# Kernel tuning notes

Measured on AMD Instinct MI355X. Metric: run time of the kernel, lower is better.

Reference implementation:

```python
import jax, jax.numpy as jnp
import numpy as np

N = 100000   # nodes
E = 400000   # edges
R = 237      # relations
D = 200      # feature dim (dims=[200,200,200])
B = 4096     # triple batch
L = 2        # num GAT layers
ALPHA = 0.01 # leaky-relu slope


def setup_inputs() -> dict:
    key = jax.random.key(0)
    ks = jax.random.split(key, 11)
    return dict(
        ent_embed=jax.random.normal(ks[0], (N, D), jnp.float32),
        rel_embed=jax.random.normal(ks[1], (R, D), jnp.float32),
        W_gat=jax.random.normal(ks[2], (L, D, D), jnp.float32) * 0.1,
        att_a=jax.random.normal(ks[3], (L, 2 * D), jnp.float32) * 0.1,
        W_hw=jax.random.normal(ks[4], (D, D), jnp.float32) * 0.1,
        b_hw=jax.random.normal(ks[5], (1, D), jnp.float32) * 0.1,
        edge_src=jax.random.randint(ks[6], (E,), 0, N),
        edge_dst=jax.random.randint(ks[7], (E,), 0, N),
        batch_h=jax.random.randint(ks[8], (B,), 0, N),
        batch_r=jax.random.randint(ks[9], (B,), 0, R),
        batch_t=jax.random.randint(ks[10], (B,), 0, N),
    )


def _gat_layer(x, W, a, src, dst):
    # x: [N,D], W: [D,D], a: [2D]
    Wh = x @ W                                  # [N,D]
    s_src = Wh @ a[:D]                          # [N] source score
    s_dst = Wh @ a[D:]                          # [N] dest score
    e = jax.nn.leaky_relu(s_src[src] + s_dst[dst], ALPHA)  # [E]
    # segment softmax over incoming edges of each destination node
    m = jax.ops.segment_max(e, dst, num_segments=N)
    m = jax.lax.stop_gradient(jnp.where(jnp.isfinite(m), m, 0.0))
    ex = jnp.exp(e - m[dst])
    denom = jax.ops.segment_sum(ex, dst, num_segments=N)
    att = ex / jnp.maximum(denom[dst], 1e-9)    # [E]
    out = jax.ops.segment_sum(att[:, None] * Wh[src], dst, num_segments=N)  # [N,D]
    return jax.nn.sigmoid(out)                  # act = torch.sigmoid, 1 head, concat=False


def reference(ent_embed, rel_embed, W_gat, att_a, W_hw, b_hw,
              edge_src, edge_dst, batch_h, batch_r, batch_t):
    x = ent_embed
    for i in range(L):
        gat_out = _gat_layer(x, W_gat[i], att_a[i], edge_src, edge_dst)
        # highway gate: sigma = sigmoid(x W + b); shared W,b across layers
        sigma = jax.nn.sigmoid(x @ W_hw + b_hw)
        x = sigma * gat_out + (1.0 - sigma) * x
    h = x[batch_h]
    r = rel_embed[batch_r]
    t = x[batch_t]
    return (h, r, t)
```

## Files before the change

kernel.cpp:

```cpp
#include <hip/hip_runtime.h>
#include <math.h>

#define NNODES 100000
#define NEDGES 400000
#define DIM    200
#define NB     4096
#define NL     2
#define ALPHA  0.01f
#define D4     (DIM/4)
#define NPAD   100096
#define KPAD   224
#define NKS    7
#define NCF    26
#define NBB    (2*NB)
#define NBLK   ((NNODES + 255) / 256)
#define SCAN_BPB 1024
#define NSB    ((NNODES + SCAN_BPB - 1) / SCAN_BPB)
#define GFULL  (NPAD / 32)
#define GEMM_TOT (2 * GFULL)
#define SLICE  ((GEMM_TOT + 3) / 4)
#define CSBLK  ((NPAD * 32) / 256)
#define HBLK   ((NEDGES + 255) / 256)
#define PREPBLK ((2 * NKS * NCF * 64 + NL * 2 * DIM + 255) / 256)
#define SCATB  ((NEDGES + 447) / 448)
#define MARKB  ((NBB + 447) / 448)
#define SGB    (NBB / 32)
#define RELB   ((NB * D4 + 447) / 448)

typedef __attribute__((ext_vector_type(8))) short short8;
typedef __attribute__((ext_vector_type(4))) float f32x4;

__device__ __forceinline__ float sigm(float v) { return 1.0f / (1.0f + expf(-v)); }
__device__ __forceinline__ unsigned short f2bf(float f) {
    unsigned u = __float_as_uint(f);
    unsigned r = u + 0x7fff + ((u >> 16) & 1);
    return (unsigned short)(r >> 16);
}
__device__ __forceinline__ float bflo(unsigned u) { return __uint_as_float(u << 16); }
__device__ __forceinline__ float bfhi(unsigned u) { return __uint_as_float(u & 0xffff0000u); }

template<int MODE>
__device__ void scan_body(const int* __restrict__ in, int* __restrict__ state,
                          int* __restrict__ ticket, int* __restrict__ o0,
                          int* __restrict__ o1, int* __restrict__ o2, int tid)
{
    __shared__ int sbid;
    __shared__ int tmp[256];
    __shared__ int sexcl;
    if (tid == 0) sbid = atomicAdd(ticket, 1);
    __syncthreads();
    int bid = sbid;
    int base = bid * SCAN_BPB + tid * 4;

    int4 v4 = make_int4(0, 0, 0, 0);
    if (tid < 256) {
        if (base + 3 < NNODES) v4 = *(const int4*)(in + base);
        else {
            if (base + 0 < NNODES) v4.x = in[base + 0];
            if (base + 1 < NNODES) v4.y = in[base + 1];
            if (base + 2 < NNODES) v4.z = in[base + 2];
        }
    }
    int s1 = v4.x + v4.y, s2 = s1 + v4.z, s3 = s2 + v4.w;

    if (tid < 256) tmp[tid] = s3;
    __syncthreads();
#pragma unroll
    for (int off = 1; off < 256; off <<= 1) {
        int t = (tid < 256 && tid >= off) ? tmp[tid - off] : 0;
        __syncthreads();
        if (tid < 256) tmp[tid] += t;
        __syncthreads();
    }
    int bexcl_t = (tid < 256) ? (tmp[tid] - s3) : 0;
    int btotal  = tmp[255];

    if (tid == 0) {
        int st = (bid == 0) ? ((2 << 30) | btotal) : ((1 << 30) | btotal);
        __hip_atomic_store(&state[bid], st, __ATOMIC_RELEASE, __HIP_MEMORY_SCOPE_AGENT);
        if (bid == 0) sexcl = 0;
    }
    if (bid > 0 && tid < 64) {
        int excl = 0;
        int pred = bid - 1;
        while (pred >= -64) {
            int idx = pred - tid;
            int s = (idx >= 0)
                ? __hip_atomic_load(&state[idx], __ATOMIC_ACQUIRE, __HIP_MEMORY_SCOPE_AGENT)
                : (2 << 30);
            int f = ((unsigned)s) >> 30;
            unsigned long long nv = __ballot(f == 0);
            unsigned long long iv = __ballot(f == 2);
            int firstnv = nv ? (__ffsll(nv) - 1) : 64;
            int firstiv = iv ? (__ffsll(iv) - 1) : 64;
            if (firstiv < firstnv) {
                int contrib = (tid <= firstiv) ? (s & 0x3FFFFFFF) : 0;
#pragma unroll
                for (int m = 32; m; m >>= 1) contrib += __shfl_xor(contrib, m, 64);
                excl += contrib;
                break;
            } else if (firstnv > 0) {
                int contrib = (tid < firstnv) ? (s & 0x3FFFFFFF) : 0;
#pragma unroll
                for (int m = 32; m; m >>= 1) contrib += __shfl_xor(contrib, m, 64);
                excl += contrib;
                pred -= firstnv;
            }
        }
        if (tid == 0) {
            __hip_atomic_store(&state[bid], (2 << 30) | (excl + btotal),
                               __ATOMIC_RELEASE, __HIP_MEMORY_SCOPE_AGENT);
            sexcl = excl;
        }
    }
    __syncthreads();
    int ex = sexcl + bexcl_t;

    if (tid < 256) {
        if (MODE == 0) {
            int4 r = make_int4(ex, ex + v4.x, ex + s1, ex + s2);
            if (base + 3 < NNODES) {
                *(int4*)(o0 + base) = r;
                *(int4*)(o1 + base) = r;
            } else {
                if (base + 0 < NNODES) { o0[base + 0] = r.x; o1[base + 0] = r.x; }
                if (base + 1 < NNODES) { o0[base + 1] = r.y; o1[base + 1] = r.y; }
                if (base + 2 < NNODES) { o0[base + 2] = r.z; o1[base + 2] = r.z; }
            }
            if (bid == NSB - 1 && tid == 0) o0[NNODES] = NEDGES;
        } else {
            int vv[4] = { v4.x, v4.y, v4.z, v4.w };
            int ee[4] = { ex, ex + v4.x, ex + s1, ex + s2 };
#pragma unroll
            for (int j = 0; j < 4; ++j) {
                int idx = base + j;
                if (idx < NNODES) {
                    if (vv[j]) { o0[ee[j]] = idx; o1[idx] = ee[j]; }
                    if (idx == NNODES - 1) *o2 = ee[j] + vv[j];
                }
            }
        }
    }
}

template<int CFBASE, int IND>
__device__ __forceinline__ void gemm_body(const unsigned short* __restrict__ Apack,
                                          const unsigned short* __restrict__ Wpack,
                                          const float* __restrict__ bhw,
                                          unsigned short* __restrict__ outb,
                                          const int* __restrict__ Lrow,
                                          const int* __restrict__ bh,
                                          const int* __restrict__ bt,
                                          int nrows, int vb, int tid)
{
    int rowbase = vb * 32;
    if (rowbase >= nrows) return;

    int w = tid >> 6;
    int l = tid & 63;
    int cgrp = l >> 4, cidx = l & 15;
    int cf0 = CFBASE + 2 * w;
    int cf1 = CFBASE + 2 * w + 1;
    int cf1l = (cf1 < NCF) ? cf1 : (NCF - 1);

    const short8* Bp = (const short8*)Wpack + l;
    short8 b0[NKS], b1[NKS];
#pragma unroll
    for (int ks = 0; ks < NKS; ++ks) {
        b0[ks] = Bp[(ks * NCF + cf0) * 64];
        b1[ks] = Bp[(ks * NCF + cf1l) * 64];
    }

    int e0 = rowbase + cidx, e1 = rowbase + 16 + cidx;
    int ar0, ar1;
    if (IND == 1) {
        ar0 = Lrow[min(e0, nrows - 1)];
        ar1 = Lrow[min(e1, nrows - 1)];
    } else if (IND == 2) {
        int c0 = min(e0, nrows - 1), c1 = min(e1, nrows - 1);
        ar0 = (c0 < NB) ? bh[c0] : bt[c0 - NB];
        ar1 = (c1 < NB) ? bh[c1] : bt[c1 - NB];
    } else { ar0 = e0; ar1 = e1; }

    const short8* Ap0 = (const short8*)(Apack + (size_t)ar0 * KPAD + cgrp * 8);
    const short8* Ap1 = (const short8*)(Apack + (size_t)ar1 * KPAD + cgrp * 8);

    f32x4 acc00 = (f32x4){0.f,0.f,0.f,0.f}, acc01 = acc00, acc10 = acc00, acc11 = acc00;

    short8 a0[2], a1[2];
    a0[0] = Ap0[0];
    a1[0] = Ap1[0];

#pragma unroll
    for (int ks = 0; ks < NKS; ++ks) {
        const int cur = ks & 1, nxt = cur ^ 1;
        if (ks + 1 < NKS) {
            a0[nxt] = Ap0[(ks + 1) * 4];
            a1[nxt] = Ap1[(ks + 1) * 4];
        }
        acc00 = __builtin_amdgcn_mfma_f32_16x16x32_bf16(a0[cur], b0[ks], acc00, 0, 0, 0);
        acc01 = __builtin_amdgcn_mfma_f32_16x16x32_bf16(a0[cur], b1[ks], acc01, 0, 0, 0);
        acc10 = __builtin_amdgcn_mfma_f32_16x16x32_bf16(a1[cur], b0[ks], acc10, 0, 0, 0);
        acc11 = __builtin_amdgcn_mfma_f32_16x16x32_bf16(a1[cur], b1[ks], acc11, 0, 0, 0);
    }

#pragma unroll
    for (int cc = 0; cc < 2; ++cc) {
        int cf = cc ? cf1 : cf0;
        if (cf >= CFBASE + 13) continue;
        int col = (cf - CFBASE) * 16 + cidx;
        if (col >= DIM) continue;
        f32x4 ar_0 = cc ? acc01 : acc00;
        f32x4 ar_1 = cc ? acc11 : acc10;
        if (CFBASE == 0) {
#pragma unroll
            for (int r = 0; r < 4; ++r) {
                int row = rowbase + cgrp * 4 + r;
                if (row < nrows) outb[(size_t)row * DIM + col] = f2bf(ar_0[r]);
                row += 16;
                if (row < nrows) outb[(size_t)row * DIM + col] = f2bf(ar_1[r]);
            }
        } else {
            float bb2 = bhw[col];
#pragma unroll
            for (int r = 0; r < 4; ++r) {
                int row = rowbase + cgrp * 4 + r;
                if (row < nrows) outb[(size_t)row * DIM + col] = f2bf(sigm(ar_0[r] + bb2));
                row += 16;
                if (row < nrows) outb[(size_t)row * DIM + col] = f2bf(sigm(ar_1[r] + bb2));
            }
        }
    }
}

__global__ __launch_bounds__(256) void zeroprep_k(int* __restrict__ deg, int* __restrict__ mask,
                                                  int* __restrict__ lbbuf,
                                                  const float* __restrict__ Wg,
                                                  const float* __restrict__ Whw,
                                                  const float* __restrict__ aa,
                                                  unsigned short* __restrict__ wp0,
                                                  unsigned short* __restrict__ wp1,
                                                  float* __restrict__ wv)
{
    int bid = blockIdx.x, tid = threadIdx.x;
    if (bid < NBLK) {
        int i = bid * 256 + tid;
        if (i < NNODES) { deg[i] = 0; mask[i] = 0; }
        if (i < 320) lbbuf[i] = 0;
        return;
    }
    int t0 = (bid - NBLK) * 256 + tid;
    const int WP = NKS * NCF * 64;
    if (t0 < 2 * WP) {
        int pk = (t0 >= WP) ? 1 : 0;
        int t = t0 - pk * WP;
        const float* Wgl = Wg + (size_t)pk * DIM * DIM;
        unsigned short* wp = pk ? wp1 : wp0;
        int l = t & 63, cf = (t >> 6) % NCF, ks = t / (NCF * 64);
        int col = (cf % 13) * 16 + (l & 15);
        const float* W = (cf < 13) ? Wgl : Whw;
        unsigned rr[4];
#pragma unroll
        for (int j = 0; j < 4; ++j) {
            int ka = ks * 32 + (l >> 4) * 8 + 2 * j;
            float fa = (ka < DIM && col < DIM) ? W[ka * DIM + col] : 0.f;
            float fb = (ka + 1 < DIM && col < DIM) ? W[(ka + 1) * DIM + col] : 0.f;
            rr[j] = (unsigned)f2bf(fa) | ((unsigned)f2bf(fb) << 16);
        }
        ((uint4*)wp)[t] = make_uint4(rr[0], rr[1], rr[2], rr[3]);
    } else {
        int u = t0 - 2 * WP;
        if (u >= NL * 2 * DIM) return;
        int l = u / (2 * DIM), sd = (u / DIM) % 2, k = u % DIM;
        const float* W = Wg + (size_t)l * DIM * DIM + (size_t)k * DIM;
        const float* av = aa + (size_t)l * 2 * DIM + sd * DIM;
        float s = 0.f;
        for (int c = 0; c < DIM; ++c) s = fmaf(W[c], av[c], s);
        wv[u] = s;
    }
}

__global__ __launch_bounds__(256) void convhist_k(const float* __restrict__ xin,
                                                  const float* __restrict__ wvl,
                                                  unsigned short* __restrict__ ap,
                                                  float* __restrict__ s_src,
                                                  float* __restrict__ s_dst,
                                                  const int* __restrict__ edst,
                                                  int* __restrict__ deg)
{
    int bid = blockIdx.x, tid = threadIdx.x;
    if (bid >= CSBLK) {
        int e = (bid - CSBLK) * 256 + tid;
        if (e < NEDGES) atomicAdd(&deg[edst[e]], 1);
        return;
    }
    int gt = bid * 256 + tid;
    int row = gt >> 5, hl = gt & 31;

    float ps = 0.f, pd = 0.f;
    if (hl < 28) {
        uint4 o = make_uint4(0u, 0u, 0u, 0u);
        if (row < NNODES && hl < 25) {
            size_t base = (size_t)row * D4 + hl * 2;
            float4 x0 = ((const float4*)xin)[base];
            float4 x1 = ((const float4*)xin)[base + 1];
            o.x = (unsigned)f2bf(x0.x) | ((unsigned)f2bf(x0.y) << 16);
            o.y = (unsigned)f2bf(x0.z) | ((unsigned)f2bf(x0.w) << 16);
            o.z = (unsigned)f2bf(x1.x) | ((unsigned)f2bf(x1.y) << 16);
            o.w = (unsigned)f2bf(x1.z) | ((unsigned)f2bf(x1.w) << 16);
            float4 s0 = ((const float4*)wvl)[hl * 2];
            float4 s1 = ((const float4*)wvl)[hl * 2 + 1];
            float4 d0 = ((const float4*)(wvl + DIM))[hl * 2];
            float4 d1 = ((const float4*)(wvl + DIM))[hl * 2 + 1];
            ps = x0.x*s0.x + x0.y*s0.y + x0.z*s0.z + x0.w*s0.w
               + x1.x*s1.x + x1.y*s1.y + x1.z*s1.z + x1.w*s1.w;
            pd = x0.x*d0.x + x0.y*d0.y + x0.z*d0.z + x0.w*d0.w
               + x1.x*d1.x + x1.y*d1.y + x1.z*d1.z + x1.w*d1.w;
        }
        ((uint4*)ap)[(size_t)row * 28 + hl] = o;
    }
#pragma unroll
    for (int m = 16; m; m >>= 1) {
        ps += __shfl_xor(ps, m, 32);
        pd += __shfl_xor(pd, m, 32);
    }
    if (hl == 0 && row < NNODES) { s_src[row] = ps; s_dst[row] = pd; }
}

template<int PHASE>
__global__ __launch_bounds__(448) void carrier_k(const int* __restrict__ sin,
                                                 int* __restrict__ state,
                                                 int* __restrict__ ticket,
                                                 int* __restrict__ so0,
                                                 int* __restrict__ so1,
                                                 int* __restrict__ so2,
                                                 const int* __restrict__ esrc,
                                                 const int* __restrict__ edst,
                                                 int* __restrict__ cursor,
                                                 int* __restrict__ csr_src,
                                                 const int* __restrict__ bh,
                                                 const int* __restrict__ bt,
                                                 const int* __restrict__ rs,
                                                 int* __restrict__ mask,
                                                 const unsigned short* __restrict__ Apack,
                                                 const unsigned short* __restrict__ Wpack,
                                                 const float* __restrict__ bhw,
                                                 unsigned short* __restrict__ whb,
                                                 unsigned short* __restrict__ sgc,
                                                 int nsmall)
{
    int bid = blockIdx.x, tid = threadIdx.x;
    if (bid < nsmall) {
        if (PHASE == 0) {
            scan_body<0>(sin, state, ticket, so0, so1, so2, tid);
        } else if (PHASE == 3) {
            scan_body<1>(sin, state, ticket, so0, so1, so2, tid);
        } else if (PHASE == 1) {
            int e = bid * 448 + tid;
            if (e < NEDGES) {
                int d = edst[e];
                int p = atomicAdd(&cursor[d], 1);
                csr_src[p] = esrc[e];
            }
        } else {
            int e = bid * 448 + tid;
            if (e < NBB) {
                int node = (e < NB) ? bh[e] : bt[e - NB];
                mask[node] = 1;
                int b = rs[node], en = rs[node + 1];
                for (int j = b; j < en; ++j) mask[csr_src[j]] = 1;
            }
        }
        return;
    }
    int vb = PHASE * SLICE + (bid - nsmall);
    if (vb >= GEMM_TOT) return;
    if (vb < GFULL)
        gemm_body<0, 0>(Apack, Wpack, bhw, whb, nullptr, nullptr, nullptr, NNODES, vb, tid);
    else
        gemm_body<13, 0>(Apack, Wpack, bhw, sgc, nullptr, nullptr, nullptr, NNODES, vb - GFULL, tid);
}

__global__ __launch_bounds__(256) void agg3c_k(const int* __restrict__ csr_src,
                                               const int* __restrict__ rs,
                                               const float* __restrict__ s_src,
                                               const float* __restrict__ s_dst,
                                               const unsigned short* __restrict__ whb,
                                               const unsigned short* __restrict__ sgc,
                                               unsigned short* __restrict__ apack,
                                               const int* __restrict__ Lrow,
                                               const int* __restrict__ nLp,
                                               const float* __restrict__ wvn,
                                               float* __restrict__ o_ssrc,
                                               float* __restrict__ o_sdst)
{
    int gt = blockIdx.x * 256 + threadIdx.x;
    int lidx = gt >> 5;
    int hl = gt & 31;
    if (lidx >= *nLp) return;
    int node = Lrow[lidx];

    int beg = rs[node], end = rs[node + 1];
    float sd = s_dst[node];

    float m = -3.4e38f;
    for (int j = beg + hl; j < end; j += 32) {
        float v = s_src[csr_src[j]] + sd;
        v = v > 0.f ? v : ALPHA * v;
        m = fmaxf(m, v);
    }
#pragma unroll
    for (int s = 16; s; s >>= 1) m = fmaxf(m, __shfl_xor(m, s, 32));
    float sum = 0.f;
    for (int j = beg + hl; j < end; j += 32) {
        float v = s_src[csr_src[j]] + sd;
        v = v > 0.f ? v : ALPHA * v;
        sum += expf(v - m);
    }
#pragma unroll
    for (int s = 16; s; s >>= 1) sum += __shfl_xor(sum, s, 32);
    float inv_ = 1.f / fmaxf(sum, 1e-9f);

    float ps = 0.f, pd = 0.f;
    if (hl < 25) {
        float av[8] = {0.f, 0.f, 0.f, 0.f, 0.f, 0.f, 0.f, 0.f};
        int j = beg;
        for (; j + 1 < end; j += 2) {
            int n0 = csr_src[j], n1 = csr_src[j + 1];
            float v0 = s_src[n0] + sd, v1 = s_src[n1] + sd;
            v0 = v0 > 0.f ? v0 : ALPHA * v0;
            v1 = v1 > 0.f ? v1 : ALPHA * v1;
            float c0 = expf(v0 - m) * inv_, c1 = expf(v1 - m) * inv_;
            uint4 w0 = ((const uint4*)whb)[(size_t)n0 * 25 + hl];
            uint4 w1 = ((const uint4*)whb)[(size_t)n1 * 25 + hl];
            av[0] = fmaf(c0, bflo(w0.x), av[0]); av[0] = fmaf(c1, bflo(w1.x), av[0]);
            av[1] = fmaf(c0, bfhi(w0.x), av[1]); av[1] = fmaf(c1, bfhi(w1.x), av[1]);
            av[2] = fmaf(c0, bflo(w0.y), av[2]); av[2] = fmaf(c1, bflo(w1.y), av[2]);
            av[3] = fmaf(c0, bfhi(w0.y), av[3]); av[3] = fmaf(c1, bfhi(w1.y), av[3]);
            av[4] = fmaf(c0, bflo(w0.z), av[4]); av[4] = fmaf(c1, bflo(w1.z), av[4]);
            av[5] = fmaf(c0, bfhi(w0.z), av[5]); av[5] = fmaf(c1, bfhi(w1.z), av[5]);
            av[6] = fmaf(c0, bflo(w0.w), av[6]); av[6] = fmaf(c1, bflo(w1.w), av[6]);
            av[7] = fmaf(c0, bfhi(w0.w), av[7]); av[7] = fmaf(c1, bfhi(w1.w), av[7]);
        }
        if (j < end) {
            int n0 = csr_src[j];
            float v0 = s_src[n0] + sd;
            v0 = v0 > 0.f ? v0 : ALPHA * v0;
            float c0 = expf(v0 - m) * inv_;
            uint4 w0 = ((const uint4*)whb)[(size_t)n0 * 25 + hl];
            av[0] = fmaf(c0, bflo(w0.x), av[0]);
            av[1] = fmaf(c0, bfhi(w0.x), av[1]);
            av[2] = fmaf(c0, bflo(w0.y), av[2]);
            av[3] = fmaf(c0, bfhi(w0.y), av[3]);
            av[4] = fmaf(c0, bflo(w0.z), av[4]);
            av[5] = fmaf(c0, bfhi(w0.z), av[5]);
            av[6] = fmaf(c0, bflo(w0.w), av[6]);
            av[7] = fmaf(c0, bfhi(w0.w), av[7]);
        }

        uint4 sv = ((const uint4*)sgc)[(size_t)node * 25 + hl];
        uint4 xv = ((const uint4*)apack)[(size_t)node * 28 + hl];
        float4 o0, o1;
        float s0;
        s0 = bflo(sv.x); o0.x = s0 * sigm(av[0]) + (1.f - s0) * bflo(xv.x);
        s0 = bfhi(sv.x); o0.y = s0 * sigm(av[1]) + (1.f - s0) * bfhi(xv.x);
        s0 = bflo(sv.y); o0.z = s0 * sigm(av[2]) + (1.f - s0) * bflo(xv.y);
        s0 = bfhi(sv.y); o0.w = s0 * sigm(av[3]) + (1.f - s0) * bfhi(xv.y);
        s0 = bflo(sv.z); o1.x = s0 * sigm(av[4]) + (1.f - s0) * bflo(xv.z);
        s0 = bfhi(sv.z); o1.y = s0 * sigm(av[5]) + (1.f - s0) * bfhi(xv.z);
        s0 = bflo(sv.w); o1.z = s0 * sigm(av[6]) + (1.f - s0) * bflo(xv.w);
        s0 = bfhi(sv.w); o1.w = s0 * sigm(av[7]) + (1.f - s0) * bfhi(xv.w);

        unsigned r0 = (unsigned)f2bf(o0.x) | ((unsigned)f2bf(o0.y) << 16);
        unsigned r1 = (unsigned)f2bf(o0.z) | ((unsigned)f2bf(o0.w) << 16);
        unsigned r2 = (unsigned)f2bf(o1.x) | ((unsigned)f2bf(o1.y) << 16);
        unsigned r3 = (unsigned)f2bf(o1.z) | ((unsigned)f2bf(o1.w) << 16);
        ((uint4*)apack)[(size_t)node * 28 + hl] = make_uint4(r0, r1, r2, r3);

        float4 ws0 = ((const float4*)wvn)[hl * 2];
        float4 ws1 = ((const float4*)wvn)[hl * 2 + 1];
        float4 wd0 = ((const float4*)(wvn + DIM))[hl * 2];
        float4 wd1 = ((const float4*)(wvn + DIM))[hl * 2 + 1];
        ps = o0.x*ws0.x + o0.y*ws0.y + o0.z*ws0.z + o0.w*ws0.w
           + o1.x*ws1.x + o1.y*ws1.y + o1.z*ws1.z + o1.w*ws1.w;
        pd = o0.x*wd0.x + o0.y*wd0.y + o0.z*wd0.z + o0.w*wd0.w
           + o1.x*wd1.x + o1.y*wd1.y + o1.z*wd1.z + o1.w*wd1.w;
    }
#pragma unroll
    for (int s = 16; s; s >>= 1) {
        ps += __shfl_xor(ps, s, 32);
        pd += __shfl_xor(pd, s, 32);
    }
    if (hl == 0) { o_ssrc[node] = ps; o_sdst[node] = pd; }
}

__global__ __launch_bounds__(448) void l1pack_k(const unsigned short* __restrict__ Apack,
                                                const unsigned short* __restrict__ Wpack1,
                                                const float* __restrict__ bhw,
                                                unsigned short* __restrict__ whc,
                                                unsigned short* __restrict__ sgbatch,
                                                const int* __restrict__ Lrow,
                                                const int* __restrict__ nLp,
                                                const int* __restrict__ bh,
                                                const int* __restrict__ bt,
                                                const float* __restrict__ rel,
                                                const int* __restrict__ br,
                                                float* __restrict__ out)
{
    int bid = blockIdx.x, tid = threadIdx.x;
    if (bid < GFULL) {
        gemm_body<0, 1>(Apack, Wpack1, bhw, whc, Lrow, nullptr, nullptr, *nLp, bid, tid);
    } else if (bid < GFULL + SGB) {
        gemm_body<13, 2>(Apack, Wpack1, bhw, sgbatch, nullptr, bh, bt, NBB, bid - GFULL, tid);
    } else {
        int u = (bid - GFULL - SGB) * 448 + tid;
        if (u < NB * D4) {
            int row = u / D4, c = u - row * D4;
            ((float4*)out)[(size_t)(NB + row) * D4 + c] =
                ((const float4*)rel)[(size_t)br[row] * D4 + c];
        }
    }
}

__global__ __launch_bounds__(256) void agg4_k(const int* __restrict__ csr_src,
                                              const int* __restrict__ rs,
                                              const float* __restrict__ s_src,
                                              const float* __restrict__ s_dst,
                                              const unsigned short* __restrict__ whc,
                                              const int* __restrict__ inv,
                                              const unsigned short* __restrict__ sgbatch,
                                              const unsigned short* __restrict__ apack,
                                              const int* __restrict__ bh,
                                              const int* __restrict__ bt,
                                              float* __restrict__ out)
{
    int gt = blockIdx.x * 256 + threadIdx.x;
    int e = gt >> 5;
    int hl = gt & 31;
    if (e >= NBB) return;
    int node = (e < NB) ? bh[e] : bt[e - NB];
    int orow = (e < NB) ? e : (2 * NB + (e - NB));

    int beg = rs[node], end = rs[node + 1];
    float sd = s_dst[node];

    float m = -3.4e38f;
    for (int j = beg + hl; j < end; j += 32) {
        float v = s_src[csr_src[j]] + sd;
        v = v > 0.f ? v : ALPHA * v;
        m = fmaxf(m, v);
    }
#pragma unroll
    for (int s = 16; s; s >>= 1) m = fmaxf(m, __shfl_xor(m, s, 32));
    float sum = 0.f;
    for (int j = beg + hl; j < end; j += 32) {
        float v = s_src[csr_src[j]] + sd;
        v = v > 0.f ? v : ALPHA * v;
        sum += expf(v - m);
    }
#pragma unroll
    for (int s = 16; s; s >>= 1) sum += __shfl_xor(sum, s, 32);
    float inv_ = 1.f / fmaxf(sum, 1e-9f);

    if (hl < 25) {
        float av[8] = {0.f, 0.f, 0.f, 0.f, 0.f, 0.f, 0.f, 0.f};
        int j = beg;
        for (; j + 1 < end; j += 2) {
            int n0 = csr_src[j], n1 = csr_src[j + 1];
            float v0 = s_src[n0] + sd, v1 = s_src[n1] + sd;
            v0 = v0 > 0.f ? v0 : ALPHA * v0;
            v1 = v1 > 0.f ? v1 : ALPHA * v1;
            float c0 = expf(v0 - m) * inv_, c1 = expf(v1 - m) * inv_;
            uint4 w0 = ((const uint4*)whc)[(size_t)inv[n0] * 25 + hl];
            uint4 w1 = ((const uint4*)whc)[(size_t)inv[n1] * 25 + hl];
            av[0] = fmaf(c0, bflo(w0.x), av[0]); av[0] = fmaf(c1, bflo(w1.x), av[0]);
            av[1] = fmaf(c0, bfhi(w0.x), av[1]); av[1] = fmaf(c1, bfhi(w1.x), av[1]);
            av[2] = fmaf(c0, bflo(w0.y), av[2]); av[2] = fmaf(c1, bflo(w1.y), av[2]);
            av[3] = fmaf(c0, bfhi(w0.y), av[3]); av[3] = fmaf(c1, bfhi(w1.y), av[3]);
            av[4] = fmaf(c0, bflo(w0.z), av[4]); av[4] = fmaf(c1, bflo(w1.z), av[4]);
            av[5] = fmaf(c0, bfhi(w0.z), av[5]); av[5] = fmaf(c1, bfhi(w1.z), av[5]);
            av[6] = fmaf(c0, bflo(w0.w), av[6]); av[6] = fmaf(c1, bflo(w1.w), av[6]);
            av[7] = fmaf(c0, bfhi(w0.w), av[7]); av[7] = fmaf(c1, bfhi(w1.w), av[7]);
        }
        if (j < end) {
            int n0 = csr_src[j];
            float v0 = s_src[n0] + sd;
            v0 = v0 > 0.f ? v0 : ALPHA * v0;
            float c0 = expf(v0 - m) * inv_;
            uint4 w0 = ((const uint4*)whc)[(size_t)inv[n0] * 25 + hl];
            av[0] = fmaf(c0, bflo(w0.x), av[0]);
            av[1] = fmaf(c0, bfhi(w0.x), av[1]);
            av[2] = fmaf(c0, bflo(w0.y), av[2]);
            av[3] = fmaf(c0, bfhi(w0.y), av[3]);
            av[4] = fmaf(c0, bflo(w0.z), av[4]);
            av[5] = fmaf(c0, bfhi(w0.z), av[5]);
            av[6] = fmaf(c0, bflo(w0.w), av[6]);
            av[7] = fmaf(c0, bfhi(w0.w), av[7]);
        }

        uint4 sv = ((const uint4*)sgbatch)[(size_t)e * 25 + hl];
        uint4 xv = ((const uint4*)apack)[(size_t)node * 28 + hl];
        float4 o0, o1;
        float s0;
        s0 = bflo(sv.x); o0.x = s0 * sigm(av[0]) + (1.f - s0) * bflo(xv.x);
        s0 = bfhi(sv.x); o0.y = s0 * sigm(av[1]) + (1.f - s0) * bfhi(xv.x);
        s0 = bflo(sv.y); o0.z = s0 * sigm(av[2]) + (1.f - s0) * bflo(xv.y);
        s0 = bfhi(sv.y); o0.w = s0 * sigm(av[3]) + (1.f - s0) * bfhi(xv.y);
        s0 = bflo(sv.z); o1.x = s0 * sigm(av[4]) + (1.f - s0) * bflo(xv.z);
        s0 = bfhi(sv.z); o1.y = s0 * sigm(av[5]) + (1.f - s0) * bfhi(xv.z);
        s0 = bflo(sv.w); o1.z = s0 * sigm(av[6]) + (1.f - s0) * bflo(xv.w);
        s0 = bfhi(sv.w); o1.w = s0 * sigm(av[7]) + (1.f - s0) * bfhi(xv.w);

        size_t base = (size_t)orow * D4 + hl * 2;
        ((float4*)out)[base]     = o0;
        ((float4*)out)[base + 1] = o1;
    }
}

extern "C" void kernel_launch(void* const* d_in, const int* in_sizes, int n_in,
                              void* d_out, int out_size, void* d_ws, size_t ws_size,
                              hipStream_t stream)
{
    const float* ent = (const float*)d_in[0];
    const float* rel = (const float*)d_in[1];
    const float* Wg  = (const float*)d_in[2];
    const float* aa  = (const float*)d_in[3];
    const float* Whw = (const float*)d_in[4];
    const float* bhw = (const float*)d_in[5];
    const int* esrc  = (const int*)d_in[6];
    const int* edst  = (const int*)d_in[7];
    const int* bh    = (const int*)d_in[8];
    const int* br    = (const int*)d_in[9];
    const int* bt    = (const int*)d_in[10];
    float* out = (float*)d_out;

    char* p = (char*)d_ws;
    auto carve = [&](size_t bytes) { char* r = p; p += (bytes + 63) & ~(size_t)63; return r; };
    unsigned short* whb     = (unsigned short*)carve((size_t)NNODES * DIM * 2);
    unsigned short* whc     = (unsigned short*)carve((size_t)NNODES * DIM * 2);
    unsigned short* sgc     = (unsigned short*)carve((size_t)NNODES * DIM * 2);
    unsigned short* apack   = (unsigned short*)carve((size_t)NPAD * KPAD * 2);
    unsigned short* sgbatch = (unsigned short*)carve((size_t)NBB * DIM * 2);
    unsigned short* wp0     = (unsigned short*)carve((size_t)NKS * NCF * 64 * 16);
    unsigned short* wp1     = (unsigned short*)carve((size_t)NKS * NCF * 64 * 16);
    float* wv    = (float*)carve(NL * 2 * DIM * 4);
    float* ss0   = (float*)carve(NNODES * 4);
    float* sd0   = (float*)carve(NNODES * 4);
    float* ss1   = (float*)carve(NNODES * 4);
    float* sd1   = (float*)carve(NNODES * 4);
    int* deg     = (int*)carve(NNODES * 4);
    int* rs      = (int*)carve((NNODES + 1) * 4);
    int* cursor  = (int*)carve(NNODES * 4);
    int* csr_src = (int*)carve(NEDGES * 4);
    int* mask    = (int*)carve(NNODES * 4);
    int* Lrow    = (int*)carve(NNODES * 4);
    int* inv     = (int*)carve(NNODES * 4);
    int* lbbuf   = (int*)carve(320 * 4);
    int* nLp     = (int*)carve(64);

    int* st0   = lbbuf;
    int* st1   = lbbuf + 128;
    int* tick0 = lbbuf + 256;
    int* tick1 = lbbuf + 257;

    zeroprep_k<<<NBLK + PREPBLK, 256, 0, stream>>>(deg, mask, lbbuf,
                                                   Wg, Whw, aa, wp0, wp1, wv);

    convhist_k<<<CSBLK + HBLK, 256, 0, stream>>>(ent, wv, apack, ss0, sd0, edst, deg);

    carrier_k<0><<<NSB + SLICE, 448, 0, stream>>>(deg, st0, tick0, rs, cursor, nullptr,
        esrc, edst, cursor, csr_src, bh, bt, rs, mask, apack, wp0, bhw, whb, sgc, NSB);
    carrier_k<1><<<SCATB + SLICE, 448, 0, stream>>>(nullptr, nullptr, nullptr, nullptr, nullptr, nullptr,
        esrc, edst, cursor, csr_src, bh, bt, rs, mask, apack, wp0, bhw, whb, sgc, SCATB);
    carrier_k<2><<<MARKB + SLICE, 448, 0, stream>>>(nullptr, nullptr, nullptr, nullptr, nullptr, nullptr,
        esrc, edst, cursor, csr_src, bh, bt, rs, mask, apack, wp0, bhw, whb, sgc, MARKB);
    carrier_k<3><<<NSB + SLICE, 448, 0, stream>>>(mask, st1, tick1, Lrow, inv, nLp,
        esrc, edst, cursor, csr_src, bh, bt, rs, mask, apack, wp0, bhw, whb, sgc, NSB);

    agg3c_k<<<(NNODES * 32) / 256, 256, 0, stream>>>(csr_src, rs, ss0, sd0, whb, sgc,
                                                     apack, Lrow, nLp, wv + 2 * DIM, ss1, sd1);

    l1pack_k<<<GFULL + SGB + RELB, 448, 0, stream>>>(apack, wp1, bhw, whc, sgbatch,
                                                     Lrow, nLp, bh, bt, rel, br, out);

    agg4_k<<<(NBB * 32) / 256, 256, 0, stream>>>(csr_src, rs, ss1, sd1, whc, inv,
                                                 sgbatch, apack, bh, bt, out);
}
```

Measured before the change: 227.5 us.

## Split carrier kernels apart and compute highway gate only for live rows

Replaces the four carrier kernels, which piggybacked GEMM slices onto the scan, scatter and mark phases, with standalone scan, scatter and mark kernels followed by dedicated GEMM launches. The Wh GEMM still covers all rows. The sigmoid-gate GEMM now runs only over the compacted set of nodes that layer 0 actually needs (Lrow/nLp) and indexes sgc by compacted id. This cuts gate GEMM work but gives up the overlap of GEMM with the latency-bound graph-build phases and adds launches. Grid size is still GFULL, so most gate blocks exit early.

```diff
diff --git a/kernel.cpp b/kernel.cpp
--- a/kernel.cpp
+++ b/kernel.cpp
@@ -17,13 +17,9 @@
 #define SCAN_BPB 1024
 #define NSB    ((NNODES + SCAN_BPB - 1) / SCAN_BPB)
 #define GFULL  (NPAD / 32)
-#define GEMM_TOT (2 * GFULL)
-#define SLICE  ((GEMM_TOT + 3) / 4)
 #define CSBLK  ((NPAD * 32) / 256)
 #define HBLK   ((NEDGES + 255) / 256)
 #define PREPBLK ((2 * NKS * NCF * 64 + NL * 2 * DIM + 255) / 256)
-#define SCATB  ((NEDGES + 447) / 448)
-#define MARKB  ((NBB + 447) / 448)
 #define SGB    (NBB / 32)
 #define RELB   ((NB * D4 + 447) / 448)
 
@@ -40,39 +36,40 @@
 __device__ __forceinline__ float bfhi(unsigned u) { return __uint_as_float(u & 0xffff0000u); }
 
 template<int MODE>
-__device__ void scan_body(const int* __restrict__ in, int* __restrict__ state,
-                          int* __restrict__ ticket, int* __restrict__ o0,
-                          int* __restrict__ o1, int* __restrict__ o2, int tid)
+__global__ __launch_bounds__(256) void scanlb_k(const int* __restrict__ in,
+                                                int* __restrict__ state,
+                                                int* __restrict__ ticket,
+                                                int* __restrict__ o0,
+                                                int* __restrict__ o1,
+                                                int* __restrict__ o2)
 {
     __shared__ int sbid;
     __shared__ int tmp[256];
     __shared__ int sexcl;
+    int tid = threadIdx.x;
     if (tid == 0) sbid = atomicAdd(ticket, 1);
     __syncthreads();
     int bid = sbid;
     int base = bid * SCAN_BPB + tid * 4;
 
     int4 v4 = make_int4(0, 0, 0, 0);
-    if (tid < 256) {
-        if (base + 3 < NNODES) v4 = *(const int4*)(in + base);
-        else {
-            if (base + 0 < NNODES) v4.x = in[base + 0];
-            if (base + 1 < NNODES) v4.y = in[base + 1];
-            if (base + 2 < NNODES) v4.z = in[base + 2];
-        }
+    if (base + 3 < NNODES) v4 = *(const int4*)(in + base);
+    else {
+        if (base + 0 < NNODES) v4.x = in[base + 0];
+        if (base + 1 < NNODES) v4.y = in[base + 1];
+        if (base + 2 < NNODES) v4.z = in[base + 2];
     }
     int s1 = v4.x + v4.y, s2 = s1 + v4.z, s3 = s2 + v4.w;
 
-    if (tid < 256) tmp[tid] = s3;
-    __syncthreads();
+    tmp[tid] = s3; __syncthreads();
 #pragma unroll
     for (int off = 1; off < 256; off <<= 1) {
-        int t = (tid < 256 && tid >= off) ? tmp[tid - off] : 0;
+        int t = (tid >= off) ? tmp[tid - off] : 0;
         __syncthreads();
-        if (tid < 256) tmp[tid] += t;
+        tmp[tid] += t;
         __syncthreads();
     }
-    int bexcl_t = (tid < 256) ? (tmp[tid] - s3) : 0;
+    int bexcl_t = tmp[tid] - s3;
     int btotal  = tmp[255];
 
     if (tid == 0) {
@@ -116,121 +113,51 @@
     __syncthreads();
     int ex = sexcl + bexcl_t;
 
-    if (tid < 256) {
-        if (MODE == 0) {
-            int4 r = make_int4(ex, ex + v4.x, ex + s1, ex + s2);
-            if (base + 3 < NNODES) {
-                *(int4*)(o0 + base) = r;
-                *(int4*)(o1 + base) = r;
-            } else {
-                if (base + 0 < NNODES) { o0[base + 0] = r.x; o1[base + 0] = r.x; }
-                if (base + 1 < NNODES) { o0[base + 1] = r.y; o1[base + 1] = r.y; }
-                if (base + 2 < NNODES) { o0[base + 2] = r.z; o1[base + 2] = r.z; }
+    if (MODE == 0) {
+        int4 r = make_int4(ex, ex + v4.x, ex + s1, ex + s2);
+        if (base + 3 < NNODES) {
+            *(int4*)(o0 + base) = r;
+            *(int4*)(o1 + base) = r;
+        } else {
+            if (base + 0 < NNODES) { o0[base + 0] = r.x; o1[base + 0] = r.x; }
+            if (base + 1 < NNODES) { o0[base + 1] = r.y; o1[base + 1] = r.y; }
+            if (base + 2 < NNODES) { o0[base + 2] = r.z; o1[base + 2] = r.z; }
+        }
+        if (bid == NSB - 1 && tid == 0) o0[NNODES] = NEDGES;
+    } else {
+        int vv[4] = { v4.x, v4.y, v4.z, v4.w };
+        int ee[4] = { ex, ex + v4.x, ex + s1, ex + s2 };
+#pragma unroll
+        for (int j = 0; j < 4; ++j) {
+            int idx = base + j;
+            if (idx < NNODES) {
+                if (vv[j]) { o0[ee[j]] = idx; o1[idx] = ee[j]; }
+                if (idx == NNODES - 1) *o2 = ee[j] + vv[j];
             }
-            if (bid == NSB - 1 && tid == 0) o0[NNODES] = NEDGES;
-        } else {
-            int vv[4] = { v4.x, v4.y, v4.z, v4.w };
-            int ee[4] = { ex, ex + v4.x, ex + s1, ex + s2 };
-#pragma unroll
-            for (int j = 0; j < 4; ++j) {
-                int idx = base + j;
-                if (idx < NNODES) {
-                    if (vv[j]) { o0[ee[j]] = idx; o1[idx] = ee[j]; }
-                    if (idx == NNODES - 1) *o2 = ee[j] + vv[j];
-                }
-            }
-        }
-    }
-}
-
-template<int CFBASE, int IND>
-__device__ __forceinline__ void gemm_body(const unsigned short* __restrict__ Apack,
-                                          const unsigned short* __restrict__ Wpack,
-                                          const float* __restrict__ bhw,
-                                          unsigned short* __restrict__ outb,
-                                          const int* __restrict__ Lrow,
-                                          const int* __restrict__ bh,
-                                          const int* __restrict__ bt,
-                                          int nrows, int vb, int tid)
-{
-    int rowbase = vb * 32;
-    if (rowbase >= nrows) return;
-
-    int w = tid >> 6;
-    int l = tid & 63;
-    int cgrp = l >> 4, cidx = l & 15;
-    int cf0 = CFBASE + 2 * w;
-    int cf1 = CFBASE + 2 * w + 1;
-    int cf1l = (cf1 < NCF) ? cf1 : (NCF - 1);
-
-    const short8* Bp = (const short8*)Wpack + l;
-    short8 b0[NKS], b1[NKS];
-#pragma unroll
-    for (int ks = 0; ks < NKS; ++ks) {
-        b0[ks] = Bp[(ks * NCF + cf0) * 64];
-        b1[ks] = Bp[(ks * NCF + cf1l) * 64];
-    }
-
-    int e0 = rowbase + cidx, e1 = rowbase + 16 + cidx;
-    int ar0, ar1;
-    if (IND == 1) {
-        ar0 = Lrow[min(e0, nrows - 1)];
-        ar1 = Lrow[min(e1, nrows - 1)];
-    } else if (IND == 2) {
-        int c0 = min(e0, nrows - 1), c1 = min(e1, nrows - 1);
-        ar0 = (c0 < NB) ? bh[c0] : bt[c0 - NB];
-        ar1 = (c1 < NB) ? bh[c1] : bt[c1 - NB];
-    } else { ar0 = e0; ar1 = e1; }
-
-    const short8* Ap0 = (const short8*)(Apack + (size_t)ar0 * KPAD + cgrp * 8);
-    const short8* Ap1 = (const short8*)(Apack + (size_t)ar1 * KPAD + cgrp * 8);
-
-    f32x4 acc00 = (f32x4){0.f,0.f,0.f,0.f}, acc01 = acc00, acc10 = acc00, acc11 = acc00;
-
-    short8 a0[2], a1[2];
-    a0[0] = Ap0[0];
-    a1[0] = Ap1[0];
-
-#pragma unroll
-    for (int ks = 0; ks < NKS; ++ks) {
-        const int cur = ks & 1, nxt = cur ^ 1;
-        if (ks + 1 < NKS) {
-            a0[nxt] = Ap0[(ks + 1) * 4];
-            a1[nxt] = Ap1[(ks + 1) * 4];
-        }
-        acc00 = __builtin_amdgcn_mfma_f32_16x16x32_bf16(a0[cur], b0[ks], acc00, 0, 0, 0);
-        acc01 = __builtin_amdgcn_mfma_f32_16x16x32_bf16(a0[cur], b1[ks], acc01, 0, 0, 0);
-        acc10 = __builtin_amdgcn_mfma_f32_16x16x32_bf16(a1[cur], b0[ks], acc10, 0, 0, 0);
-        acc11 = __builtin_amdgcn_mfma_f32_16x16x32_bf16(a1[cur], b1[ks], acc11, 0, 0, 0);
-    }
-
-#pragma unroll
-    for (int cc = 0; cc < 2; ++cc) {
-        int cf = cc ? cf1 : cf0;
-        if (cf >= CFBASE + 13) continue;
-        int col = (cf - CFBASE) * 16 + cidx;
-        if (col >= DIM) continue;
-        f32x4 ar_0 = cc ? acc01 : acc00;
-        f32x4 ar_1 = cc ? acc11 : acc10;
-        if (CFBASE == 0) {
-#pragma unroll
-            for (int r = 0; r < 4; ++r) {
-                int row = rowbase + cgrp * 4 + r;
-                if (row < nrows) outb[(size_t)row * DIM + col] = f2bf(ar_0[r]);
-                row += 16;
-                if (row < nrows) outb[(size_t)row * DIM + col] = f2bf(ar_1[r]);
-            }
-        } else {
-            float bb2 = bhw[col];
-#pragma unroll
-            for (int r = 0; r < 4; ++r) {
-                int row = rowbase + cgrp * 4 + r;
-                if (row < nrows) outb[(size_t)row * DIM + col] = f2bf(sigm(ar_0[r] + bb2));
-                row += 16;
-                if (row < nrows) outb[(size_t)row * DIM + col] = f2bf(sigm(ar_1[r] + bb2));
-            }
-        }
-    }
+        }
+    }
+}
+
+__global__ void scatter_k(const int* __restrict__ src, const int* __restrict__ dst,
+                          int* __restrict__ cursor, int* __restrict__ csr_src)
+{
+    int e = blockIdx.x * blockDim.x + threadIdx.x;
+    if (e >= NEDGES) return;
+    int d = dst[e];
+    int p = atomicAdd(&cursor[d], 1);
+    csr_src[p] = src[e];
+}
+
+__global__ void mark_k(const int* __restrict__ bh, const int* __restrict__ bt,
+                       const int* __restrict__ rs, const int* __restrict__ csr_src,
+                       int* __restrict__ mask)
+{
+    int e = blockIdx.x * 256 + threadIdx.x;
+    if (e >= NBB) return;
+    int node = (e < NB) ? bh[e] : bt[e - NB];
+    mask[node] = 1;
+    int b = rs[node], en = rs[node + 1];
+    for (int j = b; j < en; ++j) mask[csr_src[j]] = 1;
 }
 
 __global__ __launch_bounds__(256) void zeroprep_k(int* __restrict__ deg, int* __restrict__ mask,
@@ -280,21 +207,21 @@
     }
 }
 
-__global__ __launch_bounds__(256) void convhist_k(const float* __restrict__ xin,
-                                                  const float* __restrict__ wvl,
-                                                  unsigned short* __restrict__ ap,
-                                                  float* __restrict__ s_src,
-                                                  float* __restrict__ s_dst,
-                                                  const int* __restrict__ edst,
-                                                  int* __restrict__ deg)
+__global__ __launch_bounds__(256) void convscorehist_k(const float* __restrict__ xin,
+                                                       const float* __restrict__ wvl,
+                                                       unsigned short* __restrict__ ap,
+                                                       float* __restrict__ s_src,
+                                                       float* __restrict__ s_dst,
+                                                       const int* __restrict__ edst,
+                                                       int* __restrict__ deg)
 {
     int bid = blockIdx.x, tid = threadIdx.x;
-    if (bid >= CSBLK) {
-        int e = (bid - CSBLK) * 256 + tid;
+    if (bid < HBLK) {
+        int e = bid * 256 + tid;
         if (e < NEDGES) atomicAdd(&deg[edst[e]], 1);
         return;
     }
-    int gt = bid * 256 + tid;
+    int gt = (bid - HBLK) * 256 + tid;
     int row = gt >> 5, hl = gt & 31;
 
     float ps = 0.f, pd = 0.f;
@@ -327,58 +254,113 @@
     if (hl == 0 && row < NNODES) { s_src[row] = ps; s_dst[row] = pd; }
 }
 
-template<int PHASE>
-__global__ __launch_bounds__(448) void carrier_k(const int* __restrict__ sin,
-                                                 int* __restrict__ state,
-                                                 int* __restrict__ ticket,
-                                                 int* __restrict__ so0,
-                                                 int* __restrict__ so1,
-                                                 int* __restrict__ so2,
-                                                 const int* __restrict__ esrc,
-                                                 const int* __restrict__ edst,
-                                                 int* __restrict__ cursor,
-                                                 int* __restrict__ csr_src,
-                                                 const int* __restrict__ bh,
-                                                 const int* __restrict__ bt,
-                                                 const int* __restrict__ rs,
-                                                 int* __restrict__ mask,
-                                                 const unsigned short* __restrict__ Apack,
-                                                 const unsigned short* __restrict__ Wpack,
-                                                 const float* __restrict__ bhw,
-                                                 unsigned short* __restrict__ whb,
-                                                 unsigned short* __restrict__ sgc,
-                                                 int nsmall)
-{
-    int bid = blockIdx.x, tid = threadIdx.x;
-    if (bid < nsmall) {
-        if (PHASE == 0) {
-            scan_body<0>(sin, state, ticket, so0, so1, so2, tid);
-        } else if (PHASE == 3) {
-            scan_body<1>(sin, state, ticket, so0, so1, so2, tid);
-        } else if (PHASE == 1) {
-            int e = bid * 448 + tid;
-            if (e < NEDGES) {
-                int d = edst[e];
-                int p = atomicAdd(&cursor[d], 1);
-                csr_src[p] = esrc[e];
+template<int CFBASE, int IND>
+__device__ __forceinline__ void gemm_body(const unsigned short* __restrict__ Apack,
+                                          const unsigned short* __restrict__ Wpack,
+                                          const float* __restrict__ bhw,
+                                          unsigned short* __restrict__ outb,
+                                          const int* __restrict__ Lrow,
+                                          const int* __restrict__ bh,
+                                          const int* __restrict__ bt,
+                                          int nrows, int vb, int tid)
+{
+    int rowbase = vb * 32;
+    if (rowbase >= nrows) return;
+
+    int w = tid >> 6;
+    int l = tid & 63;
+    int cgrp = l >> 4, cidx = l & 15;
+    int cf0 = CFBASE + 2 * w;
+    int cf1 = CFBASE + 2 * w + 1;
+    int cf1l = (cf1 < NCF) ? cf1 : (NCF - 1);
+
+    const short8* Bp = (const short8*)Wpack + l;
+    short8 b0[NKS], b1[NKS];
+#pragma unroll
+    for (int ks = 0; ks < NKS; ++ks) {
+        b0[ks] = Bp[(ks * NCF + cf0) * 64];
+        b1[ks] = Bp[(ks * NCF + cf1l) * 64];
+    }
+
+    int e0 = rowbase + cidx, e1 = rowbase + 16 + cidx;
+    int ar0, ar1;
+    if (IND == 1) {
+        ar0 = Lrow[min(e0, nrows - 1)];
+        ar1 = Lrow[min(e1, nrows - 1)];
+    } else if (IND == 2) {
+        int c0 = min(e0, nrows - 1), c1 = min(e1, nrows - 1);
+        ar0 = (c0 < NB) ? bh[c0] : bt[c0 - NB];
+        ar1 = (c1 < NB) ? bh[c1] : bt[c1 - NB];
+    } else { ar0 = e0; ar1 = e1; }
+
+    const short8* Ap0 = (const short8*)(Apack + (size_t)ar0 * KPAD + cgrp * 8);
+    const short8* Ap1 = (const short8*)(Apack + (size_t)ar1 * KPAD + cgrp * 8);
+
+    f32x4 acc00 = (f32x4){0.f,0.f,0.f,0.f}, acc01 = acc00, acc10 = acc00, acc11 = acc00;
+
+    short8 a0[2], a1[2];
+    a0[0] = Ap0[0];
+    a1[0] = Ap1[0];
+
+#pragma unroll
+    for (int ks = 0; ks < NKS; ++ks) {
+        const int cur = ks & 1, nxt = cur ^ 1;
+        if (ks + 1 < NKS) {
+            a0[nxt] = Ap0[(ks + 1) * 4];
+            a1[nxt] = Ap1[(ks + 1) * 4];
+        }
+        acc00 = __builtin_amdgcn_mfma_f32_16x16x32_bf16(a0[cur], b0[ks], acc00, 0, 0, 0);
+        acc01 = __builtin_amdgcn_mfma_f32_16x16x32_bf16(a0[cur], b1[ks], acc01, 0, 0, 0);
+        acc10 = __builtin_amdgcn_mfma_f32_16x16x32_bf16(a1[cur], b0[ks], acc10, 0, 0, 0);
+        acc11 = __builtin_amdgcn_mfma_f32_16x16x32_bf16(a1[cur], b1[ks], acc11, 0, 0, 0);
+    }
+
+#pragma unroll
+    for (int cc = 0; cc < 2; ++cc) {
+        int cf = cc ? cf1 : cf0;
+        if (cf >= CFBASE + 13) continue;
+        int col = (cf - CFBASE) * 16 + cidx;
+        if (col >= DIM) continue;
+        f32x4 ar_0 = cc ? acc01 : acc00;
+        f32x4 ar_1 = cc ? acc11 : acc10;
+        if (CFBASE == 0) {
+#pragma unroll
+            for (int r = 0; r < 4; ++r) {
+                int row = rowbase + cgrp * 4 + r;
+                if (row < nrows) outb[(size_t)row * DIM + col] = f2bf(ar_0[r]);
+                row += 16;
+                if (row < nrows) outb[(size_t)row * DIM + col] = f2bf(ar_1[r]);
             }
         } else {
-            int e = bid * 448 + tid;
-            if (e < NBB) {
-                int node = (e < NB) ? bh[e] : bt[e - NB];
-                mask[node] = 1;
-                int b = rs[node], en = rs[node + 1];
-                for (int j = b; j < en; ++j) mask[csr_src[j]] = 1;
+            float bb2 = bhw[col];
+#pragma unroll
+            for (int r = 0; r < 4; ++r) {
+                int row = rowbase + cgrp * 4 + r;
+                if (row < nrows) outb[(size_t)row * DIM + col] = f2bf(sigm(ar_0[r] + bb2));
+                row += 16;
+                if (row < nrows) outb[(size_t)row * DIM + col] = f2bf(sigm(ar_1[r] + bb2));
             }
         }
-        return;
-    }
-    int vb = PHASE * SLICE + (bid - nsmall);
-    if (vb >= GEMM_TOT) return;
-    if (vb < GFULL)
-        gemm_body<0, 0>(Apack, Wpack, bhw, whb, nullptr, nullptr, nullptr, NNODES, vb, tid);
-    else
-        gemm_body<13, 0>(Apack, Wpack, bhw, sgc, nullptr, nullptr, nullptr, NNODES, vb - GFULL, tid);
+    }
+}
+
+__global__ __launch_bounds__(448) void gemm_whb_k(const unsigned short* __restrict__ Apack,
+                                                  const unsigned short* __restrict__ Wpack,
+                                                  unsigned short* __restrict__ whb)
+{
+    gemm_body<0, 0>(Apack, Wpack, nullptr, whb, nullptr, nullptr, nullptr,
+                    NNODES, blockIdx.x, threadIdx.x);
+}
+
+__global__ __launch_bounds__(448) void gemm_sgc_k(const unsigned short* __restrict__ Apack,
+                                                  const unsigned short* __restrict__ Wpack,
+                                                  const float* __restrict__ bhw,
+                                                  unsigned short* __restrict__ sgc,
+                                                  const int* __restrict__ Lrow,
+                                                  const int* __restrict__ nLp)
+{
+    gemm_body<13, 1>(Apack, Wpack, bhw, sgc, Lrow, nullptr, nullptr,
+                     *nLp, blockIdx.x, threadIdx.x);
 }
 
 __global__ __launch_bounds__(256) void agg3c_k(const int* __restrict__ csr_src,
@@ -458,7 +440,7 @@
             av[7] = fmaf(c0, bfhi(w0.w), av[7]);
         }
 
-        uint4 sv = ((const uint4*)sgc)[(size_t)node * 25 + hl];
+        uint4 sv = ((const uint4*)sgc)[(size_t)lidx * 25 + hl];
         uint4 xv = ((const uint4*)apack)[(size_t)node * 28 + hl];
         float4 o0, o1;
         float s0;
@@ -666,16 +648,15 @@
     zeroprep_k<<<NBLK + PREPBLK, 256, 0, stream>>>(deg, mask, lbbuf,
                                                    Wg, Whw, aa, wp0, wp1, wv);
 
-    convhist_k<<<CSBLK + HBLK, 256, 0, stream>>>(ent, wv, apack, ss0, sd0, edst, deg);
-
-    carrier_k<0><<<NSB + SLICE, 448, 0, stream>>>(deg, st0, tick0, rs, cursor, nullptr,
-        esrc, edst, cursor, csr_src, bh, bt, rs, mask, apack, wp0, bhw, whb, sgc, NSB);
-    carrier_k<1><<<SCATB + SLICE, 448, 0, stream>>>(nullptr, nullptr, nullptr, nullptr, nullptr, nullptr,
-        esrc, edst, cursor, csr_src, bh, bt, rs, mask, apack, wp0, bhw, whb, sgc, SCATB);
-    carrier_k<2><<<MARKB + SLICE, 448, 0, stream>>>(nullptr, nullptr, nullptr, nullptr, nullptr, nullptr,
-        esrc, edst, cursor, csr_src, bh, bt, rs, mask, apack, wp0, bhw, whb, sgc, MARKB);
-    carrier_k<3><<<NSB + SLICE, 448, 0, stream>>>(mask, st1, tick1, Lrow, inv, nLp,
-        esrc, edst, cursor, csr_src, bh, bt, rs, mask, apack, wp0, bhw, whb, sgc, NSB);
+    convscorehist_k<<<HBLK + CSBLK, 256, 0, stream>>>(ent, wv, apack, ss0, sd0, edst, deg);
+
+    scanlb_k<0><<<NSB, 256, 0, stream>>>(deg, st0, tick0, rs, cursor, nullptr);
+    scatter_k<<<(NEDGES + 255) / 256, 256, 0, stream>>>(esrc, edst, cursor, csr_src);
+    mark_k<<<(NBB + 255) / 256, 256, 0, stream>>>(bh, bt, rs, csr_src, mask);
+    scanlb_k<1><<<NSB, 256, 0, stream>>>(mask, st1, tick1, Lrow, inv, nLp);
+
+    gemm_whb_k<<<GFULL, 448, 0, stream>>>(apack, wp0, whb);
+    gemm_sgc_k<<<GFULL, 448, 0, stream>>>(apack, wp0, bhw, sgc, Lrow, nLp);
 
     agg3c_k<<<(NNODES * 32) / 256, 256, 0, stream>>>(csr_src, rs, ss0, sd0, whb, sgc,
                                                      apack, Lrow, nLp, wv + 2 * DIM, ss1, sd1);
```

New measurement: 207.9 us. -8.6%, faster.
